# Optimization experiments

Measured on AMD Instinct MI355X. Metric: run time of the kernel, lower is better.

The kernel has to match this reference:

```python
import jax, jax.numpy as jnp
import numpy as np

IN_FEATURES = 4096
PADDED_DIM = 4096           # == in_features -> pad and crop are identity
K_HALF = PADDED_DIM // 2 + 1  # 2049
K_KEEP = 1024               # low-pass mask: keep first K coefficients
BATCH = 8192


def _half_clean(H_real, H_imag):
    """Masked half-spectrum with real DC and Nyquist bins (padded_dim even)."""
    mask = (jnp.arange(K_HALF) < K_KEEP).astype(H_real.dtype)
    mask = jax.lax.stop_gradient(mask)
    hr = H_real * mask
    hi = H_imag * mask
    hi = hi.at[0].set(0.0)    # DC bin real
    hi = hi.at[-1].set(0.0)   # Nyquist bin real (padded_dim even, k_half > 1)
    return hr + 1j * hi


def setup_inputs() -> dict:
    key = jax.random.key(0)
    k1, k2, k3, k4 = jax.random.split(key, 4)
    x = jax.random.normal(k1, (BATCH, IN_FEATURES), jnp.float32)
    H_real = jax.random.normal(k2, (K_HALF,), jnp.float32) * 0.1
    H_imag = jax.random.normal(k3, (K_HALF,), jnp.float32) * 0.1
    bias = jax.random.normal(k4, (PADDED_DIM,), jnp.float32) * 0.1
    return {"x": x, "H_real": H_real, "H_imag": H_imag, "bias": bias}


def reference(x, H_real, H_imag, bias):
    # in_features == padded_dim, so no pad/crop needed.
    Xf = jnp.fft.rfft(x, axis=-1, norm="ortho")           # [B, K_HALF] complex64
    Yf = Xf * _half_clean(H_real, H_imag)                  # elementwise spectral multiply
    y = jnp.fft.irfft(Yf, n=PADDED_DIM, axis=-1, norm="ortho")  # [B, PADDED_DIM]
    y = y + bias[None, :]                                  # vector_bias=True
    return y
```

## Files before the change

### kernel.cpp

```cpp
#include <hip/hip_runtime.h>
#include <math.h>

#define NFEAT 4096
#define M     2048
#define THREADS 256
#define ROWS_PER_WG 4

#define SWZ(i) ((i) ^ (((i) >> 4) & 15))
#define TWPHYS(e) ((e) ^ (((e) >> 4) & 15))

__device__ __forceinline__ float2 cmul(float2 a, float2 b){
    return make_float2(a.x*b.x - a.y*b.y, a.x*b.y + a.y*b.x);
}
__device__ __forceinline__ float2 cadd(float2 a, float2 b){ return make_float2(a.x+b.x, a.y+b.y); }
__device__ __forceinline__ float2 csub(float2 a, float2 b){ return make_float2(a.x-b.x, a.y-b.y); }

template<int SIGN>
__device__ __forceinline__ float2 tw2048(const float2* __restrict__ twq, int tt){
    int e = (tt & 511) << 1;
    float2 w = twq[TWPHYS(e)];
    if (tt & 512)  w = make_float2(w.y, -w.x);
    if (tt & 1024) w = make_float2(-w.x, -w.y);
    if (SIGN > 0)  w.y = -w.y;
    return w;
}

template<int SIGN>
__device__ __forceinline__ void fft4(float2& a0, float2& a1, float2& a2, float2& a3){
    float2 t0 = cadd(a0,a2), t1 = csub(a0,a2);
    float2 t2 = cadd(a1,a3), t3 = csub(a1,a3);
    float2 r3 = (SIGN < 0) ? make_float2(t3.y, -t3.x) : make_float2(-t3.y, t3.x);
    a0 = cadd(t0,t2); a2 = csub(t0,t2);
    a1 = cadd(t1,r3); a3 = csub(t1,r3);
}

template<int SIGN>
__device__ __forceinline__ void fft8(float2 v[8]){
    const float C = 0.70710678118654752440f;
    float2 e0=v[0], e1=v[2], e2=v[4], e3=v[6];
    float2 o0=v[1], o1=v[3], o2=v[5], o3=v[7];
    fft4<SIGN>(e0,e1,e2,e3);
    fft4<SIGN>(o0,o1,o2,o3);
    float2 w1 = make_float2( C, (SIGN<0) ? -C : C);
    float2 w3 = make_float2(-C, (SIGN<0) ? -C : C);
    float2 o1w = cmul(o1, w1);
    float2 o2w = (SIGN<0) ? make_float2(o2.y, -o2.x) : make_float2(-o2.y, o2.x);
    float2 o3w = cmul(o3, w3);
    v[0]=cadd(e0,o0);  v[4]=csub(e0,o0);
    v[1]=cadd(e1,o1w); v[5]=csub(e1,o1w);
    v[2]=cadd(e2,o2w); v[6]=csub(e2,o2w);
    v[3]=cadd(e3,o3w); v[7]=csub(e3,o3w);
}

template<int SIGN, int NS>
__device__ __forceinline__ void stage8(const float2* __restrict__ src, float2* __restrict__ dst,
                                       const float2* __restrict__ twq, int j){
    const int m  = j & (NS - 1);
    const int tb = m * (M / (NS * 8));
    float2 v[8];
#pragma unroll
    for (int r = 0; r < 8; ++r){
        float2 a = src[SWZ(j + 256*r)];
        if (NS == 1 || r == 0) v[r] = a;
        else                   v[r] = cmul(a, tw2048<SIGN>(twq, tb * r));
    }
    fft8<SIGN>(v);
    const int idxD = ((j - m) << 3) + m;
#pragma unroll
    for (int r = 0; r < 8; ++r)
        dst[SWZ(idxD + NS*r)] = v[r];
}

extern "C" __global__ void __launch_bounds__(THREADS)
rfft_circ_kernel(const float* __restrict__ x,
                 const float* __restrict__ Hr,
                 const float* __restrict__ Hi,
                 const float* __restrict__ bias,
                 float* __restrict__ out)
{
    __shared__ float2 bufA[M];
    __shared__ float2 bufB[M];
    __shared__ float2 twq[1024];

    const int t = threadIdx.x;

    for (int i = t; i < 1024; i += THREADS){
        float s, c;
        sincosf(-6.2831853071795864769f * (float)i * (1.0f/4096.0f), &s, &c);
        twq[TWPHYS(i)] = make_float2(c, s);
    }
    __syncthreads();

#pragma unroll 1
    for (int rr = 0; rr < ROWS_PER_WG; ++rr){
        const int row = blockIdx.x * ROWS_PER_WG + rr;
        const float2* xr2 = (const float2*)(x + (size_t)row * NFEAT);

        {
            float2 v[8];
#pragma unroll
            for (int r = 0; r < 8; ++r) v[r] = xr2[t + 256*r];
            fft8<-1>(v);
            const int idxD = t << 3;
#pragma unroll
            for (int r = 0; r < 8; ++r) bufB[SWZ(idxD + r)] = v[r];
        }
        __syncthreads();

        stage8<-1,8 >(bufB, bufA, twq, t); __syncthreads();
        stage8<-1,64>(bufA, bufB, twq, t); __syncthreads();

#pragma unroll
        for (int h = 0; h < 2; ++h){
            const int j = t + 256*h;
            float2 v0 = bufB[SWZ(j)];
            float2 v1 = cmul(bufB[SWZ(j +  512)], tw2048<-1>(twq, j));
            float2 v2 = cmul(bufB[SWZ(j + 1024)], tw2048<-1>(twq, 2*j));
            float2 v3 = cmul(bufB[SWZ(j + 1536)], tw2048<-1>(twq, 3*j));
            fft4<-1>(v0,v1,v2,v3);
            bufA[SWZ(j)]        = v0;
            bufA[SWZ(j +  512)] = v1;
            bufA[SWZ(j + 1024)] = v2;
            bufA[SWZ(j + 1536)] = v3;
        }
        __syncthreads();

#pragma unroll
        for (int q = 0; q < 4; ++q){
            int k = t + THREADS*q;
            if (k == 0){
                float2 z0 = bufA[SWZ(0)];
                float X0 = z0.x + z0.y;
                float Y0 = X0 * Hr[0];
                bufB[SWZ(0)]    = make_float2(0.5f*Y0, 0.5f*Y0);
                bufB[SWZ(1024)] = make_float2(0.f, 0.f);
            } else {
                float2 zk = bufA[SWZ(k)];
                float2 zm = bufA[SWZ(2048 - k)];
                float2 w  = twq[TWPHYS(k)];
                float2 A = make_float2(0.5f*(zk.x + zm.x), 0.5f*(zk.y - zm.y));
                float2 B = make_float2(0.5f*(zk.x - zm.x), 0.5f*(zk.y + zm.y));
                float2 wB = cmul(w, B);
                float2 X = make_float2(A.x + wB.y, A.y - wB.x);
                float2 H = make_float2(Hr[k], Hi[k]);
                float2 Y = cmul(X, H);
                float2 f1 = make_float2(1.f + w.y,  w.x);
                float2 f2 = make_float2(1.f - w.y,  w.x);
                float2 Yc = make_float2(Y.x, -Y.y);
                float2 zy1 = cmul(Y,  f1);
                float2 zy2 = cmul(Yc, f2);
                bufB[SWZ(k)]        = make_float2(0.5f*zy1.x, 0.5f*zy1.y);
                bufB[SWZ(2048 - k)] = make_float2(0.5f*zy2.x, 0.5f*zy2.y);
            }
        }
        __syncthreads();

        stage8<1,1 >(bufB, bufA, twq, t); __syncthreads();
        stage8<1,8 >(bufA, bufB, twq, t); __syncthreads();
        stage8<1,64>(bufB, bufA, twq, t); __syncthreads();

        float2* yr2 = (float2*)(out + (size_t)row * NFEAT);
        const float2* br2 = (const float2*)bias;
        const float inv = (1.0f/2048.0f);
#pragma unroll
        for (int h = 0; h < 2; ++h){
            const int j = t + 256*h;
            float2 v0 = bufA[SWZ(j)];
            float2 v1 = cmul(bufA[SWZ(j +  512)], tw2048<1>(twq, j));
            float2 v2 = cmul(bufA[SWZ(j + 1024)], tw2048<1>(twq, 2*j));
            float2 v3 = cmul(bufA[SWZ(j + 1536)], tw2048<1>(twq, 3*j));
            fft4<1>(v0,v1,v2,v3);
            float2 vv[4] = {v0,v1,v2,v3};
#pragma unroll
            for (int r = 0; r < 4; ++r){
                int mo = j + 512*r;
                float2 b = br2[mo];
                float2 o;
                o.x = fmaf(vv[r].x, inv, b.x);
                o.y = fmaf(vv[r].y, inv, b.y);
                yr2[mo] = o;
            }
        }
    }
}

extern "C" void kernel_launch(void* const* d_in, const int* in_sizes, int n_in,
                              void* d_out, int out_size, void* d_ws, size_t ws_size,
                              hipStream_t stream) {
    const float* x    = (const float*)d_in[0];
    const float* Hr   = (const float*)d_in[1];
    const float* Hi   = (const float*)d_in[2];
    const float* bias = (const float*)d_in[3];
    float* out        = (float*)d_out;

    const int n_rows = in_sizes[0] / NFEAT;
    dim3 grid(n_rows / ROWS_PER_WG), block(THREADS);
    hipLaunchKernelGGL(rfft_circ_kernel, grid, block, 0, stream,
                       x, Hr, Hi, bias, out);
}
```

Before: 271.9 us.

## Prefetch next row, precompute spectral filter, fuse post-processing into first inverse stage

The next row's input is now loaded into registers during the current row's forward FFT, so the global load latency hides behind LDS work. The per-bin filter, combined with the post-processing factors, is precomputed once per workgroup as G. The spectral multiply is fused into the first inverse radix-8 stage, which removes one LDS pass and one barrier. Twiddles are now derived by repeated complex multiplication from a single table entry instead of one table lookup each, trading LDS reads for ALU work and some float rounding error.

```diff
diff --git a/kernel.cpp b/kernel.cpp
--- a/kernel.cpp
+++ b/kernel.cpp
@@ -12,18 +12,11 @@
 __device__ __forceinline__ float2 cmul(float2 a, float2 b){
     return make_float2(a.x*b.x - a.y*b.y, a.x*b.y + a.y*b.x);
 }
+__device__ __forceinline__ float2 cmul_conja(float2 a, float2 b){
+    return make_float2(a.x*b.x + a.y*b.y, a.x*b.y - a.y*b.x);
+}
 __device__ __forceinline__ float2 cadd(float2 a, float2 b){ return make_float2(a.x+b.x, a.y+b.y); }
 __device__ __forceinline__ float2 csub(float2 a, float2 b){ return make_float2(a.x-b.x, a.y-b.y); }
-
-template<int SIGN>
-__device__ __forceinline__ float2 tw2048(const float2* __restrict__ twq, int tt){
-    int e = (tt & 511) << 1;
-    float2 w = twq[TWPHYS(e)];
-    if (tt & 512)  w = make_float2(w.y, -w.x);
-    if (tt & 1024) w = make_float2(-w.x, -w.y);
-    if (SIGN > 0)  w.y = -w.y;
-    return w;
-}
 
 template<int SIGN>
 __device__ __forceinline__ void fft4(float2& a0, float2& a1, float2& a2, float2& a3){
@@ -56,22 +49,117 @@
 __device__ __forceinline__ void stage8(const float2* __restrict__ src, float2* __restrict__ dst,
                                        const float2* __restrict__ twq, int j){
     const int m  = j & (NS - 1);
-    const int tb = m * (M / (NS * 8));
     float2 v[8];
 #pragma unroll
-    for (int r = 0; r < 8; ++r){
-        float2 a = src[SWZ(j + 256*r)];
-        if (NS == 1 || r == 0) v[r] = a;
-        else                   v[r] = cmul(a, tw2048<SIGN>(twq, tb * r));
+    for (int r = 0; r < 8; ++r) v[r] = src[SWZ(j + 256*r)];
+    {
+        float2 wb = twq[TWPHYS(m * (M / (NS * 4)))];
+        if (SIGN > 0) wb.y = -wb.y;
+        float2 w = wb;
+        v[1] = cmul(v[1], w);
+#pragma unroll
+        for (int r = 2; r < 8; ++r){ w = cmul(w, wb); v[r] = cmul(v[r], w); }
     }
     fft8<SIGN>(v);
     const int idxD = ((j - m) << 3) + m;
 #pragma unroll
-    for (int r = 0; r < 8; ++r)
-        dst[SWZ(idxD + NS*r)] = v[r];
-}
-
-extern "C" __global__ void __launch_bounds__(THREADS)
+    for (int r = 0; r < 8; ++r) dst[SWZ(idxD + NS*r)] = v[r];
+}
+
+__device__ __forceinline__ void row_body(float2* __restrict__ X, float2* __restrict__ Y,
+                                         const float2* __restrict__ twq,
+                                         float2 (&pre)[8], const float2 (&G)[8],
+                                         const float2* __restrict__ xnext,
+                                         const float2* __restrict__ br2,
+                                         float2* __restrict__ yr2, int t)
+{
+    {
+        float2 v[8];
+#pragma unroll
+        for (int r = 0; r < 8; ++r) v[r] = pre[r];
+        fft8<-1>(v);
+        const int idxD = t << 3;
+#pragma unroll
+        for (int r = 0; r < 8; ++r) X[SWZ(idxD + r)] = v[r];
+    }
+    __syncthreads();
+    stage8<-1,8 >(X, Y, twq, t);  __syncthreads();
+    stage8<-1,64>(Y, X, twq, t);  __syncthreads();
+
+#pragma unroll
+    for (int h = 0; h < 2; ++h){
+        const int j = t + 256*h;
+        float2 w1 = twq[TWPHYS(2*j)];
+        float2 w2 = cmul(w1, w1);
+        float2 w3 = cmul(w2, w1);
+        float2 v0 = X[SWZ(j)];
+        float2 v1 = cmul(X[SWZ(j +  512)], w1);
+        float2 v2 = cmul(X[SWZ(j + 1024)], w2);
+        float2 v3 = cmul(X[SWZ(j + 1536)], w3);
+        fft4<-1>(v0,v1,v2,v3);
+        Y[SWZ(j)]        = v0;
+        Y[SWZ(j +  512)] = v1;
+        Y[SWZ(j + 1024)] = v2;
+        Y[SWZ(j + 1536)] = v3;
+    }
+    if (xnext){
+#pragma unroll
+        for (int r = 0; r < 8; ++r) pre[r] = xnext[t + 256*r];
+    }
+    __syncthreads();
+
+    {
+        float2 v[8];
+#pragma unroll
+        for (int r = 0; r < 8; ++r){
+            const int k  = t + 256*r;
+            const int kk = (r < 4) ? k : 2048 - k;
+            float2 zk = Y[SWZ(kk)];
+            float2 zm = Y[SWZ((2048 - kk) & 2047)];
+            float2 w  = twq[TWPHYS(kk & 1023)];
+            float2 A  = make_float2(zk.x + zm.x, zk.y - zm.y);
+            float2 B  = make_float2(zk.x - zm.x, zk.y + zm.y);
+            float2 wB = cmul(w, B);
+            float2 Xc = make_float2(A.x + wB.y, A.y - wB.x);
+            float2 vr = (r < 4) ? cmul(Xc, G[r]) : cmul_conja(Xc, G[r]);
+            if (t == 0){
+                if (r == 0){ float Y0 = (zk.x + zk.y) * G[0].x; vr = make_float2(Y0, Y0); }
+                if (r == 4){ vr = make_float2(0.f, 0.f); }
+            }
+            v[r] = vr;
+        }
+        fft8<1>(v);
+        const int idxD = t << 3;
+#pragma unroll
+        for (int r = 0; r < 8; ++r) X[SWZ(idxD + r)] = v[r];
+    }
+    __syncthreads();
+    stage8<1,8 >(X, Y, twq, t);  __syncthreads();
+    stage8<1,64>(Y, X, twq, t);  __syncthreads();
+
+    const float inv = (1.0f/8192.0f);
+#pragma unroll
+    for (int h = 0; h < 2; ++h){
+        const int j = t + 256*h;
+        float2 w1 = twq[TWPHYS(2*j)]; w1.y = -w1.y;
+        float2 w2 = cmul(w1, w1);
+        float2 w3 = cmul(w2, w1);
+        float2 v0 = X[SWZ(j)];
+        float2 v1 = cmul(X[SWZ(j +  512)], w1);
+        float2 v2 = cmul(X[SWZ(j + 1024)], w2);
+        float2 v3 = cmul(X[SWZ(j + 1536)], w3);
+        fft4<1>(v0,v1,v2,v3);
+        float2 vv[4] = {v0,v1,v2,v3};
+#pragma unroll
+        for (int r = 0; r < 4; ++r){
+            const int mo = j + 512*r;
+            float2 b = br2[mo];
+            yr2[mo] = make_float2(fmaf(vv[r].x, inv, b.x), fmaf(vv[r].y, inv, b.y));
+        }
+    }
+}
+
+extern "C" __global__ void __launch_bounds__(THREADS, 4)
 rfft_circ_kernel(const float* __restrict__ x,
                  const float* __restrict__ Hr,
                  const float* __restrict__ Hi,
@@ -83,6 +171,12 @@
     __shared__ float2 twq[1024];
 
     const int t = threadIdx.x;
+    const size_t row0 = (size_t)blockIdx.x * ROWS_PER_WG;
+    const float2* xr0 = (const float2*)(x + row0 * NFEAT);
+
+    float2 pre[8];
+#pragma unroll
+    for (int r = 0; r < 8; ++r) pre[r] = xr0[t + 256*r];
 
     for (int i = t; i < 1024; i += THREADS){
         float s, c;
@@ -91,95 +185,33 @@
     }
     __syncthreads();
 
+    float2 G[8];
+#pragma unroll
+    for (int r = 0; r < 8; ++r){
+        const int k  = t + 256*r;
+        const int kk = ((r < 4) ? k : 2048 - k) & 1023;
+        float2 w = twq[TWPHYS(kk)];
+        float2 H = make_float2(Hr[kk], Hi[kk]);
+        if (r < 4) G[r] = cmul(H, make_float2(1.f + w.y, w.x));
+        else       G[r] = cmul(make_float2(H.x, -H.y), make_float2(1.f - w.y, w.x));
+    }
+    if (t == 0){ G[0] = make_float2(2.f*Hr[0], 0.f); G[4] = make_float2(0.f, 0.f); }
+
+    const float2* br2 = (const float2*)bias;
+
 #pragma unroll 1
-    for (int rr = 0; rr < ROWS_PER_WG; ++rr){
-        const int row = blockIdx.x * ROWS_PER_WG + rr;
-        const float2* xr2 = (const float2*)(x + (size_t)row * NFEAT);
-
+    for (int rp = 0; rp < ROWS_PER_WG; rp += 2){
         {
-            float2 v[8];
-#pragma unroll
-            for (int r = 0; r < 8; ++r) v[r] = xr2[t + 256*r];
-            fft8<-1>(v);
-            const int idxD = t << 3;
-#pragma unroll
-            for (int r = 0; r < 8; ++r) bufB[SWZ(idxD + r)] = v[r];
-        }
-        __syncthreads();
-
-        stage8<-1,8 >(bufB, bufA, twq, t); __syncthreads();
-        stage8<-1,64>(bufA, bufB, twq, t); __syncthreads();
-
-#pragma unroll
-        for (int h = 0; h < 2; ++h){
-            const int j = t + 256*h;
-            float2 v0 = bufB[SWZ(j)];
-            float2 v1 = cmul(bufB[SWZ(j +  512)], tw2048<-1>(twq, j));
-            float2 v2 = cmul(bufB[SWZ(j + 1024)], tw2048<-1>(twq, 2*j));
-            float2 v3 = cmul(bufB[SWZ(j + 1536)], tw2048<-1>(twq, 3*j));
-            fft4<-1>(v0,v1,v2,v3);
-            bufA[SWZ(j)]        = v0;
-            bufA[SWZ(j +  512)] = v1;
-            bufA[SWZ(j + 1024)] = v2;
-            bufA[SWZ(j + 1536)] = v3;
-        }
-        __syncthreads();
-
-#pragma unroll
-        for (int q = 0; q < 4; ++q){
-            int k = t + THREADS*q;
-            if (k == 0){
-                float2 z0 = bufA[SWZ(0)];
-                float X0 = z0.x + z0.y;
-                float Y0 = X0 * Hr[0];
-                bufB[SWZ(0)]    = make_float2(0.5f*Y0, 0.5f*Y0);
-                bufB[SWZ(1024)] = make_float2(0.f, 0.f);
-            } else {
-                float2 zk = bufA[SWZ(k)];
-                float2 zm = bufA[SWZ(2048 - k)];
-                float2 w  = twq[TWPHYS(k)];
-                float2 A = make_float2(0.5f*(zk.x + zm.x), 0.5f*(zk.y - zm.y));
-                float2 B = make_float2(0.5f*(zk.x - zm.x), 0.5f*(zk.y + zm.y));
-                float2 wB = cmul(w, B);
-                float2 X = make_float2(A.x + wB.y, A.y - wB.x);
-                float2 H = make_float2(Hr[k], Hi[k]);
-                float2 Y = cmul(X, H);
-                float2 f1 = make_float2(1.f + w.y,  w.x);
-                float2 f2 = make_float2(1.f - w.y,  w.x);
-                float2 Yc = make_float2(Y.x, -Y.y);
-                float2 zy1 = cmul(Y,  f1);
-                float2 zy2 = cmul(Yc, f2);
-                bufB[SWZ(k)]        = make_float2(0.5f*zy1.x, 0.5f*zy1.y);
-                bufB[SWZ(2048 - k)] = make_float2(0.5f*zy2.x, 0.5f*zy2.y);
-            }
-        }
-        __syncthreads();
-
-        stage8<1,1 >(bufB, bufA, twq, t); __syncthreads();
-        stage8<1,8 >(bufA, bufB, twq, t); __syncthreads();
-        stage8<1,64>(bufB, bufA, twq, t); __syncthreads();
-
-        float2* yr2 = (float2*)(out + (size_t)row * NFEAT);
-        const float2* br2 = (const float2*)bias;
-        const float inv = (1.0f/2048.0f);
-#pragma unroll
-        for (int h = 0; h < 2; ++h){
-            const int j = t + 256*h;
-            float2 v0 = bufA[SWZ(j)];
-            float2 v1 = cmul(bufA[SWZ(j +  512)], tw2048<1>(twq, j));
-            float2 v2 = cmul(bufA[SWZ(j + 1024)], tw2048<1>(twq, 2*j));
-            float2 v3 = cmul(bufA[SWZ(j + 1536)], tw2048<1>(twq, 3*j));
-            fft4<1>(v0,v1,v2,v3);
-            float2 vv[4] = {v0,v1,v2,v3};
-#pragma unroll
-            for (int r = 0; r < 4; ++r){
-                int mo = j + 512*r;
-                float2 b = br2[mo];
-                float2 o;
-                o.x = fmaf(vv[r].x, inv, b.x);
-                o.y = fmaf(vv[r].y, inv, b.y);
-                yr2[mo] = o;
-            }
+            const int rr = rp;
+            float2* yr2 = (float2*)(out + (row0 + rr) * NFEAT);
+            const float2* xn = (rr + 1 < ROWS_PER_WG) ? xr0 + (size_t)(rr+1)*(NFEAT/2) : nullptr;
+            row_body(bufA, bufB, twq, pre, G, xn, br2, yr2, t);
+        }
+        {
+            const int rr = rp + 1;
+            float2* yr2 = (float2*)(out + (row0 + rr) * NFEAT);
+            const float2* xn = (rr + 1 < ROWS_PER_WG) ? xr0 + (size_t)(rr+1)*(NFEAT/2) : nullptr;
+            row_body(bufB, bufA, twq, pre, G, xn, br2, yr2, t);
         }
     }
 }
```

Result: slower. 394.5 us (+45.1%).
